# Performance work log

Hardware: AMD Instinct MI355X
Metric: run time of the kernel (lower is better)

## Reference

```python
import jax, jax.numpy as jnp
import numpy as np

WINDOW = 2  # window_size

def _causal_window_conv(x, W, b):
    # x: [B,T,D_in], W: [WINDOW, D_in, D_out], b: [D_out]
    # equivalent to left-padding x by WINDOW-1 zeros and a 'valid' conv
    B, T, _ = x.shape
    xp = jnp.pad(x, ((0, 0), (WINDOW - 1, 0), (0, 0)))  # [B, T+WINDOW-1, D_in]
    out = b
    for k in range(WINDOW):
        out = out + jnp.einsum('btd,de->bte', xp[:, k:k + T], W[k])
    return out  # [B,T,D_out]

def setup_inputs() -> dict:
    key = jax.random.key(0)
    ks = jax.random.split(key, 4)
    B, T, Din, Dout = 8, 4096, 256, 256
    scale = 0.05
    x = jax.random.normal(ks[0], (B, T, Din), dtype=jnp.float32)
    W_z = jax.random.normal(ks[1], (WINDOW, Din, Dout), dtype=jnp.float32) * scale
    W_f = jax.random.normal(ks[2], (WINDOW, Din, Dout), dtype=jnp.float32) * scale
    W_o = jax.random.normal(ks[3], (WINDOW, Din, Dout), dtype=jnp.float32) * scale
    b_z = jnp.zeros((Dout,), dtype=jnp.float32)
    b_f = jnp.zeros((Dout,), dtype=jnp.float32)
    b_o = jnp.zeros((Dout,), dtype=jnp.float32)
    return {"x": x, "W_z": W_z, "W_f": W_f, "W_o": W_o,
            "b_z": b_z, "b_f": b_f, "b_o": b_o}

def reference(x, W_z, W_f, W_o, b_z, b_f, b_o):
    # QRNN with fo-pooling (Bradbury et al. 2016), return_sequences=True
    z = jnp.tanh(_causal_window_conv(x, W_z, b_z))          # [B,T,D]
    f = jax.nn.sigmoid(_causal_window_conv(x, W_f, b_f))    # [B,T,D]
    o = jax.nn.sigmoid(_causal_window_conv(x, W_o, b_o))    # [B,T,D]

    def step(c, zfo):
        z_t, f_t, o_t = zfo
        c = f_t * c + (1.0 - f_t) * z_t   # fo-pooling recurrence
        h = o_t * c
        return c, h

    c0 = jnp.zeros(z.shape[::2], dtype=z.dtype)  # [B,D]
    # time-major for scan
    zfo = (z.transpose(1, 0, 2), f.transpose(1, 0, 2), o.transpose(1, 0, 2))
    _, hs = jax.lax.scan(step, c0, zfo)
    return hs.transpose(1, 0, 2)  # [B,T,D]
```

## Files before the change

### kernel.cpp

```cpp
#include <hip/hip_runtime.h>
#include <hip/hip_bf16.h>
#include <hip/hip_fp16.h>

#define BDIM 8
#define TDIM 4096
#define DDIM 256
#define MDIM (BDIM * TDIM)
#define NCHUNK 256
#define LCHUNK (TDIM / NCHUNK)

typedef _Float16 f16x8 __attribute__((ext_vector_type(8)));
typedef _Float16 f16x4 __attribute__((ext_vector_type(4)));
typedef float f32x4 __attribute__((ext_vector_type(4)));

__device__ __forceinline__ float sigmoid_(float x) {
    return 1.0f / (1.0f + __expf(-x));
}
__device__ __forceinline__ float tanh_(float x) {
    return 2.0f / (1.0f + __expf(-2.0f * x)) - 1.0f;
}

#define GLOAD_LDS16(g, l)                                                    \
    __builtin_amdgcn_global_load_lds(                                        \
        (const __attribute__((address_space(1))) void*)(g),                  \
        (__attribute__((address_space(3))) void*)(l), 16, 0, 0)

__global__ __launch_bounds__(256) void prep(
    const float* __restrict__ x, _Float16* __restrict__ xpad,
    const float* __restrict__ Wz, const float* __restrict__ Wf,
    const float* __restrict__ Wo, _Float16* __restrict__ Wt) {
    const int bx = blockIdx.x;
    if (bx < 1536) {
        const int idx = bx * 256 + threadIdx.x;
        const int n = idx & 255;
        const int kin = (idx >> 8) & 255;
        const int w = (idx >> 16) & 1;
        const int g = idx >> 17;
        const float* W = (g == 0) ? Wz : (g == 1) ? Wf : Wo;
        const float v = W[(size_t)w * 65536 + (size_t)kin * 256 + n];
        Wt[((size_t)g * 256 + n) * 512 + w * 256 + kin] = (_Float16)v;
        return;
    }
    const int bxx = bx - 1536;
    const int b = bxx / 1025;
    const int tb = bxx - b * 1025;
    const int tp = tb * 4 + (threadIdx.x >> 6);
    const int q = threadIdx.x & 63;
    if (tp > TDIM) return;
    float4 v = make_float4(0.f, 0.f, 0.f, 0.f);
    if (tp > 0)
        v = *(const float4*)(x + ((size_t)b * TDIM + tp - 1) * DDIM + q * 4);
    f16x4 h;
    h[0] = (_Float16)v.x; h[1] = (_Float16)v.y;
    h[2] = (_Float16)v.z; h[3] = (_Float16)v.w;
    *(f16x4*)(xpad + ((size_t)b * (TDIM + 1) + tp) * DDIM + q * 4) = h;
}

__global__ __launch_bounds__(256, 4) void gates_mfma(
    const _Float16* __restrict__ xpad, const _Float16* __restrict__ Wt,
    const float* __restrict__ bz, const float* __restrict__ bfv,
    const float* __restrict__ bo,
    _Float16* __restrict__ zbuf, _Float16* __restrict__ fbuf,
    _Float16* __restrict__ obuf) {
    const int hw = blockIdx.x;
    const int logical = (hw & 7) * 192 + (hw >> 3);
    const int mblk = logical / 6;
    const int rem = logical - mblk * 6;
    const int gate = rem % 3;
    const int nblk = rem / 3;
    const int m0 = mblk * 128;
    const int n0 = nblk * 128;

    const int tid = threadIdx.x;
    const int lane = tid & 63;
    const int wave = tid >> 6;
    const int wr = wave >> 1;
    const int wc = wave & 1;

    __shared__ __align__(16) char smem[32768];

    const int s = wave * 64 + lane;
    const int r1 = s >> 2;
    const int kc = (((s & 3) ^ ((s >> 3) & 3))) * 8;

    const int b = m0 >> 12;
    const int t0 = m0 & (TDIM - 1);

    const _Float16* srcA1 =
        xpad + ((size_t)b * (TDIM + 1) + t0 + r1) * DDIM + kc;
    const _Float16* srcA2 = srcA1 + (size_t)64 * DDIM;
    const _Float16* srcB1 = Wt + ((size_t)gate * 256 + n0 + r1) * 512 + kc;
    const _Float16* srcB2 = srcB1 + (size_t)64 * 512;

#define STAGE_(slot, t)                                                      \
    {                                                                        \
        char* dA = smem + (slot) * 16384 + wave * 1024;                      \
        char* dB = smem + (slot) * 16384 + 8192 + wave * 1024;               \
        GLOAD_LDS16(srcA1 + (t) * 32, dA);                                   \
        GLOAD_LDS16(srcA2 + (t) * 32, dA + 4096);                            \
        GLOAD_LDS16(srcB1 + (t) * 32, dB);                                   \
        GLOAD_LDS16(srcB2 + (t) * 32, dB + 4096);                            \
    }

    f32x4 acc[4][4] = {};
    const int am = lane & 15;
    const int kswz = (((lane >> 4) ^ ((lane >> 1) & 3))) * 8;

    STAGE_(0, 0);

#pragma unroll
    for (int t = 0; t < 16; ++t) {
        asm volatile("s_waitcnt vmcnt(0)" ::: "memory");
        __builtin_amdgcn_s_barrier();
        __builtin_amdgcn_sched_barrier(0);
        if (t < 15) STAGE_((t + 1) & 1, t + 1);

        const _Float16* Ab = (const _Float16*)(smem + (t & 1) * 16384);
        const _Float16* Bb = (const _Float16*)(smem + (t & 1) * 16384 + 8192);

        f16x8 a[4], bb[4];
#pragma unroll
        for (int i = 0; i < 4; ++i)
            a[i] = *(const f16x8*)(Ab + (wr * 64 + i * 16 + am) * 32 + kswz);
#pragma unroll
        for (int j = 0; j < 4; ++j)
            bb[j] = *(const f16x8*)(Bb + (wc * 64 + j * 16 + am) * 32 + kswz);

        asm volatile("s_waitcnt lgkmcnt(0)" ::: "memory");
        __builtin_amdgcn_sched_barrier(0);
        __builtin_amdgcn_s_setprio(1);
#pragma unroll
        for (int i = 0; i < 4; ++i)
#pragma unroll
            for (int j = 0; j < 4; ++j)
                acc[i][j] = __builtin_amdgcn_mfma_f32_16x16x32_f16(
                    bb[j], a[i], acc[i][j], 0, 0, 0);
        __builtin_amdgcn_s_setprio(0);
    }
#undef STAGE_

    const float* bias = (gate == 0) ? bz : (gate == 1) ? bfv : bo;
    _Float16* outp = (gate == 0) ? zbuf : (gate == 1) ? fbuf : obuf;
    const int nq = (lane >> 4) * 4;
#pragma unroll
    for (int i = 0; i < 4; ++i) {
        const size_t gm = (size_t)(m0 + wr * 64 + i * 16 + am);
#pragma unroll
        for (int j = 0; j < 4; ++j) {
            const int gc = n0 + wc * 64 + j * 16 + nq;
            const float4 b4 = *(const float4*)(bias + gc);
            f32x4 v = acc[i][j];
            f16x4 h;
            if (gate == 0) {
                h[0] = (_Float16)tanh_(v[0] + b4.x);
                h[1] = (_Float16)tanh_(v[1] + b4.y);
                h[2] = (_Float16)tanh_(v[2] + b4.z);
                h[3] = (_Float16)tanh_(v[3] + b4.w);
            } else {
                h[0] = (_Float16)sigmoid_(v[0] + b4.x);
                h[1] = (_Float16)sigmoid_(v[1] + b4.y);
                h[2] = (_Float16)sigmoid_(v[2] + b4.z);
                h[3] = (_Float16)sigmoid_(v[3] + b4.w);
            }
            *(f16x4*)(outp + gm * DDIM + gc) = h;
        }
    }
}

__global__ __launch_bounds__(256) void scan_pass1(
    const _Float16* __restrict__ zbuf, const _Float16* __restrict__ fbuf,
    float* __restrict__ aggA, float* __restrict__ aggB) {
    const int idx = blockIdx.x * 256 + threadIdx.x;
    const int d4 = idx & 63;
    const int chunk = (idx >> 6) & (NCHUNK - 1);
    const int b = idx >> 14;

    const size_t row0 = (size_t)b * TDIM + (size_t)chunk * LCHUNK;
    const int2* zp = (const int2*)zbuf + row0 * 64 + d4;
    const int2* fp = (const int2*)fbuf + row0 * 64 + d4;

    float A[4], c[4];
#pragma unroll
    for (int e = 0; e < 4; ++e) { A[e] = 1.0f; c[e] = 0.0f; }

    for (int i = 0; i < LCHUNK; ++i) {
        int2 fv = *fp;
        int2 zv = *zp;
        const _Float16* fh = (const _Float16*)&fv;
        const _Float16* zh = (const _Float16*)&zv;
#pragma unroll
        for (int e = 0; e < 4; ++e) {
            const float f = (float)fh[e];
            const float z = (float)zh[e];
            A[e] *= f;
            c[e] = f * c[e] + (1.0f - f) * z;
        }
        fp += 64;
        zp += 64;
    }
    ((float4*)aggA)[idx] = make_float4(A[0], A[1], A[2], A[3]);
    ((float4*)aggB)[idx] = make_float4(c[0], c[1], c[2], c[3]);
}

__global__ __launch_bounds__(256) void carry_scan(
    const float* __restrict__ aggA, const float* __restrict__ aggB,
    float* __restrict__ carry) {
    const int g = blockIdx.x * 256 + threadIdx.x;
    const int d = g & 255;
    const int b = g >> 8;
    const size_t base = (size_t)b * NCHUNK * 256 + d;

    float c = 0.0f;
    for (int ch0 = 0; ch0 < NCHUNK; ch0 += 16) {
        float A[16], Bv[16];
#pragma unroll
        for (int u = 0; u < 16; ++u) {
            const size_t p = base + (size_t)(ch0 + u) * 256;
            A[u] = aggA[p];
            Bv[u] = aggB[p];
        }
#pragma unroll
        for (int u = 0; u < 16; ++u) {
            const size_t p = base + (size_t)(ch0 + u) * 256;
            carry[p] = c;
            c = A[u] * c + Bv[u];
        }
    }
}

__global__ __launch_bounds__(256) void scan_pass2(
    const _Float16* __restrict__ zbuf, const _Float16* __restrict__ fbuf,
    const _Float16* __restrict__ obuf, const float* __restrict__ carry,
    float* __restrict__ out) {
    const int idx = blockIdx.x * 256 + threadIdx.x;
    const int d4 = idx & 63;
    const int chunk = (idx >> 6) & (NCHUNK - 1);
    const int b = idx >> 14;

    float c[4];
    const float4 c0 = ((const float4*)carry)[idx];
    c[0] = c0.x; c[1] = c0.y; c[2] = c0.z; c[3] = c0.w;

    const size_t row0 = (size_t)b * TDIM + (size_t)chunk * LCHUNK;
    const int2* zp = (const int2*)zbuf + row0 * 64 + d4;
    const int2* fp = (const int2*)fbuf + row0 * 64 + d4;
    const int2* op = (const int2*)obuf + row0 * 64 + d4;
    float4* hp = (float4*)out + row0 * 64 + d4;

    for (int i = 0; i < LCHUNK; ++i) {
        int2 fv = *fp;
        int2 zv = *zp;
        int2 ov = *op;
        const _Float16* fh = (const _Float16*)&fv;
        const _Float16* zh = (const _Float16*)&zv;
        const _Float16* oh = (const _Float16*)&ov;
        float h[4];
#pragma unroll
        for (int e = 0; e < 4; ++e) {
            const float f = (float)fh[e];
            const float z = (float)zh[e];
            c[e] = f * c[e] + (1.0f - f) * z;
            h[e] = (float)oh[e] * c[e];
        }
        *hp = make_float4(h[0], h[1], h[2], h[3]);
        fp += 64;
        zp += 64;
        op += 64;
        hp += 64;
    }
}

extern "C" void kernel_launch(void* const* d_in, const int* in_sizes, int n_in,
                              void* d_out, int out_size, void* d_ws,
                              size_t ws_size, hipStream_t stream) {
    const float* x = (const float*)d_in[0];
    const float* Wz = (const float*)d_in[1];
    const float* Wf = (const float*)d_in[2];
    const float* Wo = (const float*)d_in[3];
    const float* bz = (const float*)d_in[4];
    const float* bfv = (const float*)d_in[5];
    const float* bo = (const float*)d_in[6];
    float* out = (float*)d_out;

    char* p = (char*)d_ws;
    _Float16* xpad = (_Float16*)p;  p += (size_t)BDIM * (TDIM + 1) * DDIM * 2;
    _Float16* Wt = (_Float16*)p;    p += (size_t)3 * 256 * 512 * 2;
    _Float16* zbuf = (_Float16*)p;  p += (size_t)MDIM * DDIM * 2;
    _Float16* fbuf = (_Float16*)p;  p += (size_t)MDIM * DDIM * 2;
    _Float16* obuf = (_Float16*)p;  p += (size_t)MDIM * DDIM * 2;
    float* aggA = (float*)p;        p += (size_t)BDIM * NCHUNK * DDIM * 4;
    float* aggB = (float*)p;        p += (size_t)BDIM * NCHUNK * DDIM * 4;
    float* carry = (float*)p;

    prep<<<1536 + 1025 * BDIM, 256, 0, stream>>>(x, xpad, Wz, Wf, Wo, Wt);

    gates_mfma<<<MDIM / 128 * (DDIM / 128) * 3, 256, 0, stream>>>(
        xpad, Wt, bz, bfv, bo, zbuf, fbuf, obuf);

    scan_pass1<<<(BDIM * NCHUNK * 64) / 256, 256, 0, stream>>>(zbuf, fbuf,
                                                               aggA, aggB);
    carry_scan<<<(BDIM * DDIM) / 256, 256, 0, stream>>>(aggA, aggB, carry);
    scan_pass2<<<(BDIM * NCHUNK * 64) / 256, 256, 0, stream>>>(zbuf, fbuf,
                                                               obuf, carry, out);
}
```

Before: 162.7 us.

## Double GEMM K-tile to 64 and overlap second-half LDS reads with MFMA

```diff
diff --git a/kernel.cpp b/kernel.cpp
--- a/kernel.cpp
+++ b/kernel.cpp
@@ -56,7 +56,7 @@
     *(f16x4*)(xpad + ((size_t)b * (TDIM + 1) + tp) * DDIM + q * 4) = h;
 }
 
-__global__ __launch_bounds__(256, 4) void gates_mfma(
+__global__ __launch_bounds__(256, 2) void gates_mfma(
     const _Float16* __restrict__ xpad, const _Float16* __restrict__ Wt,
     const float* __restrict__ bz, const float* __restrict__ bfv,
     const float* __restrict__ bo,
@@ -77,55 +77,75 @@
     const int wr = wave >> 1;
     const int wc = wave & 1;
 
-    __shared__ __align__(16) char smem[32768];
+    __shared__ __align__(16) char smem[65536];
 
     const int s = wave * 64 + lane;
-    const int r1 = s >> 2;
-    const int kc = (((s & 3) ^ ((s >> 3) & 3))) * 8;
+    const int r1 = s >> 3;
+    const int kc = (((s & 7) ^ ((s >> 3) & 7))) * 8;
 
     const int b = m0 >> 12;
     const int t0 = m0 & (TDIM - 1);
 
-    const _Float16* srcA1 =
+    const _Float16* srcA =
         xpad + ((size_t)b * (TDIM + 1) + t0 + r1) * DDIM + kc;
-    const _Float16* srcA2 = srcA1 + (size_t)64 * DDIM;
-    const _Float16* srcB1 = Wt + ((size_t)gate * 256 + n0 + r1) * 512 + kc;
-    const _Float16* srcB2 = srcB1 + (size_t)64 * 512;
-
-#define STAGE_(slot, t)                                                      \
+    const _Float16* srcB = Wt + ((size_t)gate * 256 + n0 + r1) * 512 + kc;
+
+#define STAGE_(slot, kt)                                                     \
     {                                                                        \
-        char* dA = smem + (slot) * 16384 + wave * 1024;                      \
-        char* dB = smem + (slot) * 16384 + 8192 + wave * 1024;               \
-        GLOAD_LDS16(srcA1 + (t) * 32, dA);                                   \
-        GLOAD_LDS16(srcA2 + (t) * 32, dA + 4096);                            \
-        GLOAD_LDS16(srcB1 + (t) * 32, dB);                                   \
-        GLOAD_LDS16(srcB2 + (t) * 32, dB + 4096);                            \
+        char* dA = smem + (slot) * 32768 + wave * 1024;                      \
+        char* dB = smem + (slot) * 32768 + 16384 + wave * 1024;              \
+        GLOAD_LDS16(srcA + (kt) * 64, dA);                                   \
+        GLOAD_LDS16(srcA + (kt) * 64 + 32 * DDIM, dA + 4096);                \
+        GLOAD_LDS16(srcA + (kt) * 64 + 64 * DDIM, dA + 8192);                \
+        GLOAD_LDS16(srcA + (kt) * 64 + 96 * DDIM, dA + 12288);               \
+        GLOAD_LDS16(srcB + (kt) * 64, dB);                                   \
+        GLOAD_LDS16(srcB + (kt) * 64 + 32 * 512, dB + 4096);                 \
+        GLOAD_LDS16(srcB + (kt) * 64 + 64 * 512, dB + 8192);                 \
+        GLOAD_LDS16(srcB + (kt) * 64 + 96 * 512, dB + 12288);                \
     }
 
     f32x4 acc[4][4] = {};
     const int am = lane & 15;
-    const int kswz = (((lane >> 4) ^ ((lane >> 1) & 3))) * 8;
+    const int c0 = (((lane >> 4) ^ (lane & 7))) * 8;
+    const int c1 = (((4 + (lane >> 4)) ^ (lane & 7))) * 8;
 
     STAGE_(0, 0);
 
 #pragma unroll
-    for (int t = 0; t < 16; ++t) {
+    for (int t = 0; t < 8; ++t) {
         asm volatile("s_waitcnt vmcnt(0)" ::: "memory");
         __builtin_amdgcn_s_barrier();
         __builtin_amdgcn_sched_barrier(0);
-        if (t < 15) STAGE_((t + 1) & 1, t + 1);
-
-        const _Float16* Ab = (const _Float16*)(smem + (t & 1) * 16384);
-        const _Float16* Bb = (const _Float16*)(smem + (t & 1) * 16384 + 8192);
-
-        f16x8 a[4], bb[4];
+        if (t < 7) STAGE_((t + 1) & 1, t + 1);
+
+        const _Float16* Ab = (const _Float16*)(smem + (t & 1) * 32768);
+        const _Float16* Bb = Ab + 8192;
+
+        f16x8 a0[4], b0[4], a1[4], b1[4];
 #pragma unroll
         for (int i = 0; i < 4; ++i)
-            a[i] = *(const f16x8*)(Ab + (wr * 64 + i * 16 + am) * 32 + kswz);
+            a0[i] = *(const f16x8*)(Ab + (wr * 64 + i * 16 + am) * 64 + c0);
 #pragma unroll
         for (int j = 0; j < 4; ++j)
-            bb[j] = *(const f16x8*)(Bb + (wc * 64 + j * 16 + am) * 32 + kswz);
-
+            b0[j] = *(const f16x8*)(Bb + (wc * 64 + j * 16 + am) * 64 + c0);
+        __builtin_amdgcn_sched_barrier(0);
+#pragma unroll
+        for (int i = 0; i < 4; ++i)
+            a1[i] = *(const f16x8*)(Ab + (wr * 64 + i * 16 + am) * 64 + c1);
+#pragma unroll
+        for (int j = 0; j < 4; ++j)
+            b1[j] = *(const f16x8*)(Bb + (wc * 64 + j * 16 + am) * 64 + c1);
+
+        asm volatile("s_waitcnt lgkmcnt(8)" ::: "memory");
+        __builtin_amdgcn_sched_barrier(0);
+        __builtin_amdgcn_s_setprio(1);
+#pragma unroll
+        for (int i = 0; i < 4; ++i)
+#pragma unroll
+            for (int j = 0; j < 4; ++j)
+                acc[i][j] = __builtin_amdgcn_mfma_f32_16x16x32_f16(
+                    b0[j], a0[i], acc[i][j], 0, 0, 0);
+        __builtin_amdgcn_s_setprio(0);
         asm volatile("s_waitcnt lgkmcnt(0)" ::: "memory");
         __builtin_amdgcn_sched_barrier(0);
         __builtin_amdgcn_s_setprio(1);
@@ -134,7 +154,7 @@
 #pragma unroll
             for (int j = 0; j < 4; ++j)
                 acc[i][j] = __builtin_amdgcn_mfma_f32_16x16x32_f16(
-                    bb[j], a[i], acc[i][j], 0, 0, 0);
+                    b1[j], a1[i], acc[i][j], 0, 0, 0);
         __builtin_amdgcn_s_setprio(0);
     }
 #undef STAGE_
```

Measured after the change: 159.3 us. 1.02x faster.
